# Kernel tuning notes

Hardware: AMD Instinct MI355X
Metric: run time of the kernel (lower is better)

## Reference

```python
import jax, jax.numpy as jnp
import numpy as np

NUM_ENTITIES = 100000
NUM_TIMES = 10000
D = 512
DB = 768
NUM_REL = 200
NUM_BASES = 4
N_NODES = 30000
N_EDGES = 200000
B = 128
P_ENT = 64
P_TIME = 32
T_UNIQ = 2000


def setup_inputs() -> dict:
    key = jax.random.key(0)
    ks = jax.random.split(key, 32)
    n = jax.random.normal
    ri = jax.random.randint
    inp = {}
    # learned params
    inp['emb'] = n(ks[0], (NUM_ENTITIES + NUM_TIMES, D), jnp.float32) * 0.05
    sc = 1.0 / np.sqrt(D)
    inp['basis1'] = n(ks[1], (NUM_BASES, D, D), jnp.float32) * sc
    inp['att1'] = n(ks[2], (NUM_REL, NUM_BASES), jnp.float32) * 0.5
    inp['root1'] = n(ks[3], (D, D), jnp.float32) * sc
    inp['bias1'] = jnp.zeros((D,), jnp.float32)
    inp['basis2'] = n(ks[4], (NUM_BASES, D, D), jnp.float32) * sc
    inp['att2'] = n(ks[5], (NUM_REL, NUM_BASES), jnp.float32) * 0.5
    inp['root2'] = n(ks[6], (D, D), jnp.float32) * sc
    inp['bias2'] = jnp.zeros((D,), jnp.float32)
    sb = 1.0 / np.sqrt(DB)
    inp['W_lin'] = n(ks[7], (DB, D), jnp.float32) * sb
    inp['b_lin'] = jnp.zeros((D,), jnp.float32)
    inp['W_attn'] = n(ks[8], (DB, D), jnp.float32) * sb
    inp['b_attn'] = jnp.zeros((D,), jnp.float32)
    inp['W_prob'] = n(ks[9], (DB, 1), jnp.float32) * sb
    inp['b_prob'] = jnp.zeros((1,), jnp.float32)
    # forward tensor args
    inp['ques_emb_bert'] = n(ks[10], (B, DB), jnp.float32)
    inp['x_idx'] = ri(ks[11], (N_NODES,), 0, NUM_ENTITIES, jnp.int32)
    inp['edge_index'] = ri(ks[12], (2, N_EDGES), 0, N_NODES, jnp.int32)
    inp['edge_type'] = ri(ks[13], (N_EDGES,), 0, NUM_REL, jnp.int32)
    inp['start_time'] = ri(ks[14], (N_EDGES,), 0, NUM_TIMES, jnp.int32)
    inp['end_time'] = ri(ks[15], (N_EDGES,), 0, NUM_TIMES, jnp.int32)
    inp['edge_batch_idx'] = jnp.sort(ri(ks[16], (N_EDGES,), 0, B, jnp.int32))
    inp['edge_norm'] = jax.random.uniform(ks[17], (N_EDGES,), jnp.float32)
    inp['uniq_times'] = ri(ks[18], (T_UNIQ,), 0, NUM_TIMES, jnp.int32)
    # padded index vectors: positions >= count point at the appended zero row
    ent_counts = ri(ks[19], (B,), 1, P_ENT + 1, jnp.int32)
    time_counts = ri(ks[20], (B,), 1, P_TIME + 1, jnp.int32)
    pe = ri(ks[21], (B, P_ENT), 0, N_NODES, jnp.int32)
    pt = ri(ks[22], (B, P_TIME), 0, T_UNIQ, jnp.int32)
    inp['padded_ent'] = jnp.where(jnp.arange(P_ENT)[None, :] < ent_counts[:, None], pe, N_NODES)
    inp['padded_time'] = jnp.where(jnp.arange(P_TIME)[None, :] < time_counts[:, None], pt, T_UNIQ)
    inp['ent_counts'] = ent_counts
    inp['time_counts'] = time_counts
    return inp


def rgcn_layer(x, basis, att, root, bias, src, dst, etype, st_emb, et_emb, q_t, edge_norm):
    # basis decomposition: project all nodes through each basis once. [N, NB, D]
    xb = jnp.einsum('ni,bio->nbo', x, basis)
    coeff = att[etype]                                 # [E, NB]
    msg = jnp.einsum('eb,ebd->ed', coeff, xb[src])     # [E, D]
    # time gate: question-time embedding vs edge interval midpoint embedding
    gate = jax.nn.sigmoid(jnp.sum(q_t * 0.5 * (st_emb + et_emb), axis=-1))  # [E]
    msg = msg * (gate * edge_norm)[:, None]
    agg = jax.ops.segment_sum(msg, dst, num_segments=N_NODES)
    return agg + x @ root + bias


def reference(emb, basis1, att1, root1, bias1, basis2, att2, root2, bias2,
              W_lin, b_lin, W_attn, b_attn, W_prob, b_prob,
              ques_emb_bert, x_idx, edge_index, edge_type, start_time, end_time,
              edge_batch_idx, edge_norm, uniq_times, padded_ent, padded_time,
              ent_counts, time_counts):
    question_embedding = ques_emb_bert @ W_lin + b_lin                  # [B, D]
    time_for_edge_attn = (ques_emb_bert @ W_attn + b_attn)[edge_batch_idx]  # [E, D]
    st_emb = emb[start_time + NUM_ENTITIES]
    et_emb = emb[end_time + NUM_ENTITIES]
    x = emb[x_idx]                                                      # [N, D]
    src, dst = edge_index[0], edge_index[1]
    h = jax.nn.relu(rgcn_layer(x, basis1, att1, root1, bias1, src, dst, edge_type,
                               st_emb, et_emb, time_for_edge_attn, edge_norm))
    # dropout is identity in eval mode
    h = rgcn_layer(h, basis2, att2, root2, bias2, src, dst, edge_type,
                   st_emb, et_emb, time_for_edge_attn, edge_norm)       # [N, D]
    subgraph_time_emb = emb[uniq_times + NUM_ENTITIES]                  # [T_u, D]
    zero = jnp.zeros((1, D), h.dtype)
    ent_w_zeros = jnp.concatenate([h, zero], axis=0)
    time_w_zeros = jnp.concatenate([subgraph_time_emb, zero], axis=0)
    pooled_ent = jnp.sum(ent_w_zeros[padded_ent], axis=1) / ent_counts[:, None].astype(h.dtype)
    pooled_time = jnp.sum(time_w_zeros[padded_time], axis=1) / time_counts[:, None].astype(h.dtype)
    p_ent = jax.nn.sigmoid(ques_emb_bert @ W_prob + b_prob)             # [B, 1]
    pred = (question_embedding + pooled_ent * p_ent + pooled_time * (1.0 - p_ent)) / 3.0
    # batched cosine similarity against full entity+time vocab
    pred_n = pred / jnp.maximum(jnp.linalg.norm(pred, axis=-1, keepdims=True), 1e-8)
    emb_n = emb / jnp.maximum(jnp.linalg.norm(emb, axis=-1, keepdims=True), 1e-8)
    score = pred_n @ emb_n.T                                            # [B, V]
    return score * 30.0
```

## Files before the change

### kernel.cpp

```cpp
#include <hip/hip_runtime.h>

#define NUM_ENT   100000
#define NTIMES    10000
#define DD        512
#define DB        768
#define NREL      200
#define NBAS      4
#define NN        30000
#define NEDGE     200000
#define BATCH     128
#define PENT      64
#define PTIME     32
#define TUNIQ     2000
#define V_TOT     110000
#define V_PAD     110208
#define VT16      6888
#define M_PAD2    30208
#define MT2R      1888
#define KT_L      80
#define KT_E      16
#define PACKB_BLKS 1280
#define GATH_BLKS  7500

typedef __attribute__((ext_vector_type(8))) short s8v;
typedef __attribute__((ext_vector_type(4))) float f4v;

__device__ __forceinline__ unsigned short f2bf(float x){
  unsigned int u = __builtin_bit_cast(unsigned int, x);
  u += 0x7fffu + ((u >> 16) & 1u);
  return (unsigned short)(u >> 16);
}
__device__ __forceinline__ float bf2f(unsigned short h){
  unsigned int u = ((unsigned int)h) << 16;
  return __builtin_bit_cast(float, u);
}

__device__ __forceinline__ void gload16(const void* g, void* l){
  __builtin_amdgcn_global_load_lds(
      (const __attribute__((address_space(1))) void*)g,
      (__attribute__((address_space(3))) void*)l, 16, 0, 0);
}


__global__ __launch_bounds__(256) void k_prep(const float* __restrict__ emb,
    const float* __restrict__ basis1, const float* __restrict__ root1,
    const float* __restrict__ basis2, const float* __restrict__ root2,
    const int* __restrict__ x_idx,
    unsigned short* __restrict__ Bp, float* __restrict__ invn,
    unsigned short* __restrict__ B1p, unsigned short* __restrict__ B2p,
    unsigned short* __restrict__ Ap, unsigned short* __restrict__ x_rm){
  int bid = blockIdx.x;
  if (bid < VT16){
    int vt = bid;
    int wid = threadIdx.x >> 6, lane = threadIdx.x & 63;
    int vrow = vt * 16 + (lane & 15);
    float ss = 0.f;
    __shared__ float ssw[4][16];
    for (int i = 0; i < 4; ++i){
      int kt = wid + i * 4;
      int k0 = kt * 32 + (lane >> 4) * 8;
      s8v o;
      if (vrow < V_TOT){
        const float4* p = reinterpret_cast<const float4*>(emb + (size_t)vrow * DD + k0);
        float4 v0 = p[0], v1 = p[1];
        ss += v0.x*v0.x + v0.y*v0.y + v0.z*v0.z + v0.w*v0.w;
        ss += v1.x*v1.x + v1.y*v1.y + v1.z*v1.z + v1.w*v1.w;
        o[0] = (short)f2bf(v0.x); o[1] = (short)f2bf(v0.y);
        o[2] = (short)f2bf(v0.z); o[3] = (short)f2bf(v0.w);
        o[4] = (short)f2bf(v1.x); o[5] = (short)f2bf(v1.y);
        o[6] = (short)f2bf(v1.z); o[7] = (short)f2bf(v1.w);
      } else {
        #pragma unroll
        for (int j = 0; j < 8; ++j) o[j] = 0;
      }
      *reinterpret_cast<s8v*>(Bp + ((size_t)(kt * VT16 + vt) << 9) + lane * 8) = o;
    }
    ss += __shfl_xor(ss, 16);
    ss += __shfl_xor(ss, 32);
    if ((lane >> 4) == 0) ssw[wid][lane] = ss;
    __syncthreads();
    if (threadIdx.x < 16){
      float s = ssw[0][threadIdx.x] + ssw[1][threadIdx.x] + ssw[2][threadIdx.x] + ssw[3][threadIdx.x];
      int v = vt * 16 + threadIdx.x;
      invn[v] = (v < V_TOT) ? (1.0f / fmaxf(sqrtf(s), 1e-8f)) : 0.0f;
    }
  } else if (bid < VT16 + PACKB_BLKS){
    int idx = (bid - VT16) * 256 + threadIdx.x;
    int set = idx >= KT_L * 32 * 64;
    if (set) idx -= KT_L * 32 * 64;
    const float* basis = set ? basis2 : basis1;
    const float* root  = set ? root2  : root1;
    unsigned short* Bw = set ? B2p : B1p;
    int lane = idx & 63; int kt = idx >> 11;
    int k0 = kt * 32 + (lane >> 4) * 8;
    int col = ((idx >> 6) & 31) * 16 + (lane & 15);
    s8v o;
    #pragma unroll
    for (int j = 0; j < 8; ++j){
      int k = k0 + j;
      float v = (k < 2048) ? basis[(size_t)k * 512 + col] : root[(size_t)(k - 2048) * 512 + col];
      o[j] = (short)f2bf(v);
    }
    *reinterpret_cast<s8v*>(Bw + (size_t)idx * 8) = o;
  } else {
    int gb = bid - (VT16 + PACKB_BLKS);
    int w = (int)((gb * 256 + threadIdx.x) >> 6);
    int lane = threadIdx.x & 63;
    if (w >= NN) return;
    int v = x_idx[w];
    const float4* p = reinterpret_cast<const float4*>(emb + (size_t)v * 512 + lane * 8);
    float4 a = p[0], b = p[1];
    s8v x;
    x[0] = (short)f2bf(a.x); x[1] = (short)f2bf(a.y); x[2] = (short)f2bf(a.z); x[3] = (short)f2bf(a.w);
    x[4] = (short)f2bf(b.x); x[5] = (short)f2bf(b.y); x[6] = (short)f2bf(b.z); x[7] = (short)f2bf(b.w);
    *reinterpret_cast<s8v*>(x_rm + (size_t)w * 512 + lane * 8) = x;
    *reinterpret_cast<s8v*>(Ap + ((size_t)(w >> 4) * KT_L + 64 + (lane >> 2)) * 512
                               + ((w & 15) + (lane & 3) * 16) * 8) = x;
  }
}

__global__ __launch_bounds__(256) void k_small2(const float* __restrict__ ques,
    const float* __restrict__ Wl, const float* __restrict__ bl,
    const float* __restrict__ Wa, const float* __restrict__ ba,
    const float* __restrict__ Wp, const float* __restrict__ bp,
    float* __restrict__ qlin, unsigned short* __restrict__ Apq,
    float* __restrict__ pent){
  if (blockIdx.x == 32){
    int b = threadIdx.x >> 1, half = threadIdx.x & 1;
    float a = 0.f;
    int k0 = half * 384;
    for (int k = k0; k < k0 + 384; ++k)
      a = fmaf(ques[(size_t)b * DB + k], Wp[k], a);
    a += __shfl_xor(a, 1);
    if (half == 0) pent[b] = 1.f / (1.f + expf(-(a + bp[0])));
    return;
  }
  __shared__ float sq[128 * 96];
  int col = threadIdx.x & 31, bg = threadIdx.x >> 5;
  int c0 = blockIdx.x * 32;
  const float* W = (c0 < 512) ? Wl : Wa;
  int wcol = (c0 & 511) + col;
  float acc[16] = {};
  for (int k0 = 0; k0 < DB; k0 += 96){
    __syncthreads();
    for (int i = threadIdx.x; i < 128 * 96; i += 256){
      int b = i / 96, kk = i - b * 96;
      sq[i] = ques[(size_t)b * DB + k0 + kk];
    }
    __syncthreads();
    for (int kk = 0; kk < 96; kk += 4){
      float w0 = W[(size_t)(k0 + kk + 0) * 512 + wcol];
      float w1 = W[(size_t)(k0 + kk + 1) * 512 + wcol];
      float w2 = W[(size_t)(k0 + kk + 2) * 512 + wcol];
      float w3 = W[(size_t)(k0 + kk + 3) * 512 + wcol];
      #pragma unroll
      for (int bb = 0; bb < 16; ++bb){
        float4 qv = *reinterpret_cast<const float4*>(&sq[(bg * 16 + bb) * 96 + kk]);
        acc[bb] = fmaf(qv.x, w0, fmaf(qv.y, w1, fmaf(qv.z, w2, fmaf(qv.w, w3, acc[bb]))));
      }
    }
  }
  if (c0 < 512){
    #pragma unroll
    for (int bb = 0; bb < 16; ++bb)
      qlin[(size_t)(bg * 16 + bb) * 512 + wcol] = acc[bb] + bl[wcol];
  } else {
    float bb_ = ba[wcol];
    size_t base = ((size_t)bg * 16 + (wcol >> 5)) * 512
                + ((wcol >> 3) & 3) * 128 + (wcol & 7);
    #pragma unroll
    for (int bb = 0; bb < 16; ++bb){
      int w = bg * 16 + bb;
      Apq[base + (w & 15) * 8] = f2bf(acc[bb] + bb_);
    }
  }
}

__global__ __launch_bounds__(256) void k_gemm_m2(
    const unsigned short* __restrict__ A, const unsigned short* __restrict__ B,
    float* __restrict__ outf){
  __shared__ __align__(1024) short sAll[3 * 8192];
  const int Kt = KT_E;
  int tid = threadIdx.x;
  int lane = tid & 63, wid = tid >> 6;
  int wr = wid >> 1, wc = wid & 1;
  int rt0 = blockIdx.x * 8;
  int ct0 = blockIdx.y * 8;
  const unsigned short* pA0 = A + ((size_t)(rt0 + 2 * wid) * Kt) * 512 + lane * 8;
  const unsigned short* pA1 = pA0 + (size_t)Kt * 512;
  const unsigned short* pB0 = B + (size_t)(ct0 + 2 * wid) * 512 + lane * 8;
  const unsigned short* pB1 = pB0 + 512;
  size_t gbs = (size_t)VT16 * 512;
  int so = 2 * wid * 512;
  f4v acc[4][4] = {};

  auto STAGE = [&](int buf, int kt){
    short* b = &sAll[buf * 8192];
    gload16(pA0 + (size_t)kt * 512, b + so);
    gload16(pA1 + (size_t)kt * 512, b + so + 512);
    gload16(pB0 + (size_t)kt * gbs, b + 4096 + so);
    gload16(pB1 + (size_t)kt * gbs, b + 4096 + so + 512);
  };
  auto COMPUTE = [&](int buf){
    const short* base = &sAll[buf * 8192];
    s8v af[4], bfr[4];
    #pragma unroll
    for (int m = 0; m < 4; ++m) af[m] = *reinterpret_cast<const s8v*>(base + (wr * 4 + m) * 512 + lane * 8);
    #pragma unroll
    for (int n = 0; n < 4; ++n) bfr[n] = *reinterpret_cast<const s8v*>(base + 4096 + (wc * 4 + n) * 512 + lane * 8);
    #pragma unroll
    for (int m = 0; m < 4; ++m)
      #pragma unroll
      for (int n = 0; n < 4; ++n)
        acc[m][n] = __builtin_amdgcn_mfma_f32_16x16x32_bf16(af[m], bfr[n], acc[m][n], 0, 0, 0);
  };

  STAGE(0, 0);
  STAGE(1, 1);
  int cb = 0, sb = 2;
  for (int kt = 0; kt < Kt - 2; ++kt){
    STAGE(sb, kt + 2);
    asm volatile("s_waitcnt vmcnt(8)" ::: "memory");
    __builtin_amdgcn_s_barrier();
    __builtin_amdgcn_sched_barrier(0);
    COMPUTE(cb);
    __builtin_amdgcn_s_barrier();
    cb = (cb == 2) ? 0 : cb + 1;
    sb = (sb == 2) ? 0 : sb + 1;
  }
  asm volatile("s_waitcnt vmcnt(4)" ::: "memory");
  __builtin_amdgcn_s_barrier();
  __builtin_amdgcn_sched_barrier(0);
  COMPUTE(cb);
  cb = (cb == 2) ? 0 : cb + 1;
  asm volatile("s_waitcnt vmcnt(0)" ::: "memory");
  __builtin_amdgcn_s_barrier();
  __builtin_amdgcn_sched_barrier(0);
  COMPUTE(cb);

  #pragma unroll
  for (int m = 0; m < 4; ++m)
    #pragma unroll
    for (int n = 0; n < 4; ++n){
      int row0 = rt0 * 16 + (wr * 4 + m) * 16 + ((lane >> 4) * 4);
      int col  = (ct0 + wc * 4 + n) * 16 + (lane & 15);
      #pragma unroll
      for (int r = 0; r < 4; ++r){
        int rr = row0 + r;
        if (col < NTIMES) outf[(size_t)rr * NTIMES + col] = acc[m][n][r];
      }
    }
}

__global__ __launch_bounds__(256, 3) void k_score_p(
    const unsigned short* __restrict__ Apred, const unsigned short* __restrict__ Bp,
    const float* __restrict__ invn, float* __restrict__ out){
  __shared__ __align__(1024) short sAll[3 * 8192];
  const int Kt = KT_E;
  int tid = threadIdx.x;
  int lane = tid & 63, wid = tid >> 6;
  int wr = wid >> 1, wc = wid & 1;
  int kq = lane >> 4, r16 = lane & 15;
  int ct0 = blockIdx.x * 8;
  const unsigned short* pA0 = Apred + ((size_t)(2 * wid) * Kt) * 512 + lane * 8;
  const unsigned short* pA1 = pA0 + (size_t)Kt * 512;
  const unsigned short* pB0 = Bp + (size_t)(ct0 + 2 * wid) * 512 + lane * 8;
  const unsigned short* pB1 = pB0 + 512;
  size_t gbs = (size_t)VT16 * 512;
  int so = 2 * wid * 512;
  f4v acc[4][4] = {};

  auto STAGE = [&](int buf, int kt){
    short* b = &sAll[buf * 8192];
    gload16(pA0 + (size_t)kt * 512, b + so);
    gload16(pA1 + (size_t)kt * 512, b + so + 512);
    gload16(pB0 + (size_t)kt * gbs, b + 4096 + so);
    gload16(pB1 + (size_t)kt * gbs, b + 4096 + so + 512);
  };
  auto COMPUTE = [&](int buf){
    const short* base = &sAll[buf * 8192];
    s8v af[4], bfr[4];
    #pragma unroll
    for (int m = 0; m < 4; ++m) af[m] = *reinterpret_cast<const s8v*>(base + (wr * 4 + m) * 512 + lane * 8);
    #pragma unroll
    for (int n = 0; n < 4; ++n) bfr[n] = *reinterpret_cast<const s8v*>(base + 4096 + (wc * 4 + n) * 512 + lane * 8);
    #pragma unroll
    for (int m = 0; m < 4; ++m)
      #pragma unroll
      for (int n = 0; n < 4; ++n)
        acc[m][n] = __builtin_amdgcn_mfma_f32_16x16x32_bf16(af[m], bfr[n], acc[m][n], 0, 0, 0);
  };

  STAGE(0, 0);
  STAGE(1, 1);
  int cb = 0, sb = 2;
  for (int kt = 0; kt < Kt - 2; ++kt){
    STAGE(sb, kt + 2);
    asm volatile("s_waitcnt vmcnt(8)" ::: "memory");
    __builtin_amdgcn_s_barrier();
    __builtin_amdgcn_sched_barrier(0);
    COMPUTE(cb);
    __builtin_amdgcn_s_barrier();
    cb = (cb == 2) ? 0 : cb + 1;
    sb = (sb == 2) ? 0 : sb + 1;
  }
  asm volatile("s_waitcnt vmcnt(4)" ::: "memory");
  __builtin_amdgcn_s_barrier();
  __builtin_amdgcn_sched_barrier(0);
  COMPUTE(cb);
  cb = (cb == 2) ? 0 : cb + 1;
  asm volatile("s_waitcnt vmcnt(0)" ::: "memory");
  __builtin_amdgcn_s_barrier();
  __builtin_amdgcn_sched_barrier(0);
  COMPUTE(cb);

  __syncthreads();
  float* scratch = reinterpret_cast<float*>(sAll) + wid * 2176;
  int colg = ct0 * 16 + wc * 64 + r16 * 4;
  bool c_ok = colg < V_TOT;
  float4 inv4 = float4{0.f, 0.f, 0.f, 0.f};
  if (c_ok){
    inv4 = *reinterpret_cast<const float4*>(invn + colg);
    inv4.x *= 30.f; inv4.y *= 30.f; inv4.z *= 30.f; inv4.w *= 30.f;
  }
  #pragma unroll
  for (int p = 0; p < 2; ++p){
    #pragma unroll
    for (int mm = 0; mm < 2; ++mm){
      int m = p * 2 + mm;
      #pragma unroll
      for (int n = 0; n < 4; ++n)
        #pragma unroll
        for (int r = 0; r < 4; ++r)
          scratch[(mm * 16 + kq * 4 + r) * 68 + n * 16 + r16] = acc[m][n][r];
    }
    #pragma unroll
    for (int i = 0; i < 8; ++i){
      int row_r = i * 4 + kq;
      float4 v = *reinterpret_cast<const float4*>(scratch + row_r * 68 + r16 * 4);
      if (c_ok){
        float4 o;
        o.x = v.x * inv4.x; o.y = v.y * inv4.y; o.z = v.z * inv4.z; o.w = v.w * inv4.w;
        int grr = wr * 64 + p * 32 + row_r;
        *reinterpret_cast<float4*>(out + (size_t)grr * V_TOT + colg) = o;
      }
    }
  }
}

template<int MODE>
__global__ __launch_bounds__(512, 2) void k_gemm512(
    const unsigned short* __restrict__ A, const unsigned short* __restrict__ B,
    const float* __restrict__ bias, unsigned short* __restrict__ outh,
    unsigned short* __restrict__ Ap_tail){
  __shared__ __align__(1024) short sAll[3 * 20480];
  const int Kt = KT_L;
  int tid = threadIdx.x;
  int lane = tid & 63, wid = tid >> 6;
  int wr = wid >> 2, wc = wid & 3;
  int blk = blockIdx.x;
  int rt0 = blk * 8;
  const unsigned short* pA = A + ((size_t)(rt0 + wid) * Kt) * 512 + lane * 8;
  const unsigned short* pB = B + (size_t)(wid * 4) * 512 + lane * 8;
  int soA = wid * 512;
  int soB = 4096 + wid * 4 * 512;
  f4v acc[4][8] = {};

  auto STAGE = [&](int buf, int kt){
    short* b = &sAll[buf * 20480];
    gload16(pA + (size_t)kt * 512, b + soA);
    const unsigned short* pb = pB + (size_t)kt * 32 * 512;
    gload16(pb,        b + soB);
    gload16(pb +  512, b + soB +  512);
    gload16(pb + 1024, b + soB + 1024);
    gload16(pb + 1536, b + soB + 1536);
  };
  auto COMPUTE = [&](int buf){
    const short* base = &sAll[buf * 20480];
    s8v af[4], bfr[8];
    #pragma unroll
    for (int m = 0; m < 4; ++m) af[m] = *reinterpret_cast<const s8v*>(base + (wr * 4 + m) * 512 + lane * 8);
    #pragma unroll
    for (int n = 0; n < 8; ++n) bfr[n] = *reinterpret_cast<const s8v*>(base + 4096 + (wc * 8 + n) * 512 + lane * 8);
    __builtin_amdgcn_s_setprio(1);
    #pragma unroll
    for (int m = 0; m < 4; ++m)
      #pragma unroll
      for (int n = 0; n < 8; ++n)
        acc[m][n] = __builtin_amdgcn_mfma_f32_16x16x32_bf16(af[m], bfr[n], acc[m][n], 0, 0, 0);
    __builtin_amdgcn_s_setprio(0);
  };

  STAGE(0, 0);
  STAGE(1, 1);
  int cb = 0, sb = 2;
  for (int kt = 0; kt < Kt - 2; ++kt){
    STAGE(sb, kt + 2);
    asm volatile("s_waitcnt vmcnt(10)" ::: "memory");
    __builtin_amdgcn_s_barrier();
    __builtin_amdgcn_sched_barrier(0);
    COMPUTE(cb);
    __builtin_amdgcn_s_barrier();
    cb = (cb == 2) ? 0 : cb + 1;
    sb = (sb == 2) ? 0 : sb + 1;
  }
  asm volatile("s_waitcnt vmcnt(5)" ::: "memory");
  __builtin_amdgcn_s_barrier();
  __builtin_amdgcn_sched_barrier(0);
  COMPUTE(cb);
  cb = (cb == 2) ? 0 : cb + 1;
  asm volatile("s_waitcnt vmcnt(0)" ::: "memory");
  __builtin_amdgcn_s_barrier();
  __builtin_amdgcn_sched_barrier(0);
  COMPUTE(cb);

  int R0 = blk * 128 + wr * 64 + ((lane >> 4) * 4);
  int C0 = wc * 128 + (lane & 15);
  #pragma unroll
  for (int m = 0; m < 4; ++m)
    #pragma unroll
    for (int r4 = 0; r4 < 4; ++r4){
      int rr = R0 + m * 16 + r4;
      if (rr < NN){
        #pragma unroll
        for (int n = 0; n < 8; ++n){
          int col = C0 + n * 16;
          float v = acc[m][n][r4] + bias[col];
          if constexpr (MODE == 1){
            v = fmaxf(v, 0.f);
            unsigned short hv = f2bf(v);
            outh[(size_t)rr * 512 + col] = hv;
            Ap_tail[((size_t)(rr >> 4) * KT_L + 64 + (col >> 5)) * 512
                    + ((rr & 15) + ((col >> 3) & 3) * 16) * 8 + (col & 7)] = hv;
          } else {
            outh[(size_t)rr * 512 + col] = f2bf(v);
          }
        }
      }
    }
}

__global__ __launch_bounds__(256) void k_edgeprep(const int* __restrict__ ebatch,
    const int* __restrict__ st, const int* __restrict__ et,
    const float* __restrict__ enorm, const float* __restrict__ M2,
    const int* __restrict__ ei,
    float* __restrict__ we, int* __restrict__ cnt, int* __restrict__ lists){
  int e = blockIdx.x * 256 + threadIdx.x;
  if (e >= NEDGE) return;
  int b = ebatch[e];
  float s = 0.5f * (M2[(size_t)b * NTIMES + st[e]] + M2[(size_t)b * NTIMES + et[e]]);
  we[e] = (1.f / (1.f + expf(-s))) * enorm[e];
  int dst = ei[NEDGE + e];
  int slot = atomicAdd(&cnt[dst], 1);
  if (slot < 64) lists[(size_t)dst * 64 + slot] = e;
}

__global__ __launch_bounds__(256) void k_edge_agg(const unsigned short* __restrict__ xsrc,
    const int* __restrict__ ei, const int* __restrict__ etype,
    const float* __restrict__ we, const float* __restrict__ att,
    const int* __restrict__ cnt, const int* __restrict__ lists,
    unsigned short* __restrict__ Ap){
  __shared__ float satt[NREL * NBAS];
  __shared__ int sed[4][64];
  for (int i = threadIdx.x; i < NREL * NBAS; i += 256) satt[i] = att[i];
  int wid = threadIdx.x >> 6, lane = threadIdx.x & 63;
  int n = blockIdx.x * 4 + wid;
  int deg = min(cnt[n], 64);
  int eid = (lane < deg) ? lists[(size_t)n * 64 + lane] : 0x7fffffff;
  int rank = 0;
  for (int j = 0; j < 64; ++j){
    int v = __shfl(eid, j);
    rank += (v < eid) ? 1 : 0;
  }
  __syncthreads();
  if (lane < deg) sed[wid][rank] = eid;
  __syncthreads();
  float acc[NBAS][8] = {};
  if (deg > 0){
    int my_e = sed[wid][(lane < deg) ? lane : 0];
    int my_s = ei[my_e];
    int my_t = etype[my_e];
    float my_w = we[my_e];
    float c0l = my_w * satt[my_t * 4 + 0];
    float c1l = my_w * satt[my_t * 4 + 1];
    float c2l = my_w * satt[my_t * 4 + 2];
    float c3l = my_w * satt[my_t * 4 + 3];
    int s0 = __shfl(my_s, 0);
    s8v xv = *reinterpret_cast<const s8v*>(xsrc + (size_t)s0 * 512 + lane * 8);
    for (int j = 0; j < deg; ++j){
      s8v xn = xv;
      if (j + 1 < deg){
        int sn = __shfl(my_s, j + 1);
        xn = *reinterpret_cast<const s8v*>(xsrc + (size_t)sn * 512 + lane * 8);
      }
      float c0 = __shfl(c0l, j), c1 = __shfl(c1l, j);
      float c2 = __shfl(c2l, j), c3 = __shfl(c3l, j);
      #pragma unroll
      for (int jj = 0; jj < 8; ++jj){
        float x = bf2f((unsigned short)xv[jj]);
        acc[0][jj] = fmaf(c0, x, acc[0][jj]);
        acc[1][jj] = fmaf(c1, x, acc[1][jj]);
        acc[2][jj] = fmaf(c2, x, acc[2][jj]);
        acc[3][jj] = fmaf(c3, x, acc[3][jj]);
      }
      xv = xn;
    }
  }
  #pragma unroll
  for (int b = 0; b < NBAS; ++b){
    s8v o;
    #pragma unroll
    for (int jj = 0; jj < 8; ++jj) o[jj] = (short)f2bf(acc[b][jj]);
    *reinterpret_cast<s8v*>(Ap + ((size_t)(n >> 4) * KT_L + b * 16 + (lane >> 2)) * 512
                               + ((n & 15) + (lane & 3) * 16) * 8) = o;
  }
}

__global__ __launch_bounds__(256) void k_pred(const unsigned short* __restrict__ h2,
    const float* __restrict__ emb, const int* __restrict__ uniq,
    const int* __restrict__ pent_idx, const int* __restrict__ ptime_idx,
    const int* __restrict__ ent_c, const int* __restrict__ time_c,
    const float* __restrict__ qlin, const float* __restrict__ pent,
    unsigned short* __restrict__ Ap_pred){
  __shared__ float sacc[4][512];
  int b = blockIdx.x;
  int wid = threadIdx.x >> 6, lane = threadIdx.x & 63;
  float a[8] = {};
  if (wid < 2){
    for (int j = wid * 32; j < wid * 32 + 32; ++j){
      int idx = pent_idx[b * PENT + j];
      if (idx < NN){
        s8v hv = *reinterpret_cast<const s8v*>(h2 + (size_t)idx * 512 + lane * 8);
        #pragma unroll
        for (int jj = 0; jj < 8; ++jj) a[jj] += bf2f((unsigned short)hv[jj]);
      }
    }
  } else {
    for (int j = (wid - 2) * 16; j < (wid - 2) * 16 + 16; ++j){
      int ti = ptime_idx[b * PTIME + j];
      if (ti < TUNIQ){
        const float* p = emb + (size_t)(NUM_ENT + uniq[ti]) * 512 + lane * 8;
        #pragma unroll
        for (int jj = 0; jj < 8; ++jj) a[jj] += p[jj];
      }
    }
  }
  #pragma unroll
  for (int jj = 0; jj < 8; ++jj) sacc[wid][lane * 8 + jj] = a[jj];
  __syncthreads();
  if (wid == 0){
    float ce = 1.f / (float)ent_c[b], ct = 1.f / (float)time_c[b];
    float p = pent[b];
    float pr[8]; float ss = 0.f;
    #pragma unroll
    for (int jj = 0; jj < 8; ++jj){
      int i = lane * 8 + jj;
      float ae = sacc[0][i] + sacc[1][i];
      float at = sacc[2][i] + sacc[3][i];
      float v = (qlin[(size_t)b * 512 + i] + ae * ce * p + at * ct * (1.f - p)) * (1.f / 3.f);
      pr[jj] = v; ss += v * v;
    }
    ss += __shfl_xor(ss, 32); ss += __shfl_xor(ss, 16); ss += __shfl_xor(ss, 8);
    ss += __shfl_xor(ss, 4);  ss += __shfl_xor(ss, 2);  ss += __shfl_xor(ss, 1);
    float inv = 1.f / fmaxf(sqrtf(ss), 1e-8f);
    s8v o;
    #pragma unroll
    for (int jj = 0; jj < 8; ++jj) o[jj] = (short)f2bf(pr[jj] * inv);
    *reinterpret_cast<s8v*>(Ap_pred + ((size_t)((b >> 4) * KT_E + (lane >> 2)) << 9)
                                    + ((b & 15) + (lane & 3) * 16) * 8) = o;
  }
}

extern "C" void kernel_launch(void* const* d_in, const int* in_sizes, int n_in,
                              void* d_out, int out_size, void* d_ws, size_t ws_size,
                              hipStream_t stream){
  const float* emb    = (const float*)d_in[0];
  const float* basis1 = (const float*)d_in[1];
  const float* att1   = (const float*)d_in[2];
  const float* root1  = (const float*)d_in[3];
  const float* bias1  = (const float*)d_in[4];
  const float* basis2 = (const float*)d_in[5];
  const float* att2   = (const float*)d_in[6];
  const float* root2  = (const float*)d_in[7];
  const float* bias2  = (const float*)d_in[8];
  const float* W_lin  = (const float*)d_in[9];
  const float* b_lin  = (const float*)d_in[10];
  const float* W_attn = (const float*)d_in[11];
  const float* b_attn = (const float*)d_in[12];
  const float* W_prob = (const float*)d_in[13];
  const float* b_prob = (const float*)d_in[14];
  const float* ques   = (const float*)d_in[15];
  const int* x_idx    = (const int*)d_in[16];
  const int* eidx     = (const int*)d_in[17];
  const int* etype    = (const int*)d_in[18];
  const int* stime    = (const int*)d_in[19];
  const int* etime    = (const int*)d_in[20];
  const int* ebatch   = (const int*)d_in[21];
  const float* enorm  = (const float*)d_in[22];
  const int* uniq     = (const int*)d_in[23];
  const int* pent_i   = (const int*)d_in[24];
  const int* ptime_i  = (const int*)d_in[25];
  const int* ent_c    = (const int*)d_in[26];
  const int* time_c   = (const int*)d_in[27];
  float* out = (float*)d_out;

  char* w = (char*)d_ws;
  size_t off = 0;
  auto alloc = [&](size_t bytes)->char*{ char* p = w + off; off += (bytes + 255) & ~(size_t)255; return p; };
  unsigned short* Bp_emb = (unsigned short*)alloc((size_t)KT_E * VT16 * 1024);
  float*          invn   = (float*)alloc((size_t)V_PAD * 4);
  unsigned short* Ap   = (unsigned short*)alloc((size_t)MT2R * KT_L * 1024);
  unsigned short* B1p  = (unsigned short*)alloc((size_t)KT_L * 32 * 1024);
  unsigned short* B2p  = (unsigned short*)alloc((size_t)KT_L * 32 * 1024);
  char* xh_base = alloc((size_t)NN * 512 * 2 * 2);
  unsigned short* x_rm = (unsigned short*)xh_base;
  unsigned short* h1   = (unsigned short*)(xh_base + (size_t)NN * 512 * 2);
  unsigned short* h2   = (unsigned short*)xh_base;
  float* M2    = (float*)alloc((size_t)BATCH * NTIMES * 4);
  float* we    = (float*)alloc((size_t)NEDGE * 4);
  float* qlin  = (float*)alloc((size_t)BATCH * 512 * 4);
  float* pent  = (float*)alloc(1024);
  unsigned short* Apq    = (unsigned short*)alloc((size_t)8 * KT_E * 1024);
  unsigned short* Appred = (unsigned short*)alloc((size_t)8 * KT_E * 1024);
  int* cnt   = (int*)alloc((size_t)NN * 4);
  int* lists = (int*)alloc((size_t)NN * 64 * 4);
  (void)ws_size; (void)in_sizes; (void)n_in; (void)out_size;

  k_prep<<<VT16 + PACKB_BLKS + GATH_BLKS, 256, 0, stream>>>(
      emb, basis1, root1, basis2, root2, x_idx,
      Bp_emb, invn, B1p, B2p, Ap, x_rm);
  k_small2<<<33, 256, 0, stream>>>(ques, W_lin, b_lin, W_attn, b_attn, W_prob, b_prob,
                                   qlin, Apq, pent);
  k_gemm_m2<<<dim3(1, 79), 256, 0, stream>>>(Apq, Bp_emb + (size_t)6250 * 512, M2);
  hipMemsetAsync(cnt, 0, (size_t)NN * 4, stream);
  k_edgeprep<<<(NEDGE + 255) / 256, 256, 0, stream>>>(ebatch, stime, etime, enorm, M2,
                                                      eidx, we, cnt, lists);
  k_edge_agg<<<NN / 4, 256, 0, stream>>>(x_rm, eidx, etype, we, att1, cnt, lists, Ap);
  k_gemm512<1><<<236, 512, 0, stream>>>(Ap, B1p, bias1, h1, Ap);
  k_edge_agg<<<NN / 4, 256, 0, stream>>>(h1, eidx, etype, we, att2, cnt, lists, Ap);
  k_gemm512<2><<<236, 512, 0, stream>>>(Ap, B2p, bias2, h2, nullptr);
  k_pred<<<BATCH, 256, 0, stream>>>(h2, emb, uniq, pent_i, ptime_i, ent_c, time_c,
                                    qlin, pent, Appred);
  k_score_p<<<861, 256, 0, stream>>>(Appred, Bp_emb, invn, out);
}
```

Baseline: 676.9 us.

## Drop row-major activation copies and gather edge sources from tiled GEMM buffer

The gather and layer-1 GEMM no longer write separate row-major bf16 copies of the node features (x_rm and h1). Edge aggregation instead reads source rows straight from the tiled tail of the GEMM A buffer. This removes two full N×D bf16 write streams and a workspace buffer. In exchange, each edge now gathers its row as 16-byte pieces spread across 16 tiles rather than one contiguous 1 KB row, which may coalesce worse. Separately, the vocab packing step now reads embedding rows contiguously, transposes them through shared memory, and computes norms from the bf16-rounded values.

```diff
diff --git a/kernel.cpp b/kernel.cpp
--- a/kernel.cpp
+++ b/kernel.cpp
@@ -48,23 +48,21 @@
     const int* __restrict__ x_idx,
     unsigned short* __restrict__ Bp, float* __restrict__ invn,
     unsigned short* __restrict__ B1p, unsigned short* __restrict__ B2p,
-    unsigned short* __restrict__ Ap, unsigned short* __restrict__ x_rm){
+    unsigned short* __restrict__ Ap){
+  __shared__ unsigned short srow[16][520];
+  __shared__ float ssw[4][16];
   int bid = blockIdx.x;
   if (bid < VT16){
     int vt = bid;
     int wid = threadIdx.x >> 6, lane = threadIdx.x & 63;
-    int vrow = vt * 16 + (lane & 15);
-    float ss = 0.f;
-    __shared__ float ssw[4][16];
+    #pragma unroll
     for (int i = 0; i < 4; ++i){
-      int kt = wid + i * 4;
-      int k0 = kt * 32 + (lane >> 4) * 8;
+      int r = wid * 4 + i;
+      int vrow = vt * 16 + r;
       s8v o;
       if (vrow < V_TOT){
-        const float4* p = reinterpret_cast<const float4*>(emb + (size_t)vrow * DD + k0);
+        const float4* p = reinterpret_cast<const float4*>(emb + (size_t)vrow * DD + lane * 8);
         float4 v0 = p[0], v1 = p[1];
-        ss += v0.x*v0.x + v0.y*v0.y + v0.z*v0.z + v0.w*v0.w;
-        ss += v1.x*v1.x + v1.y*v1.y + v1.z*v1.z + v1.w*v1.w;
         o[0] = (short)f2bf(v0.x); o[1] = (short)f2bf(v0.y);
         o[2] = (short)f2bf(v0.z); o[3] = (short)f2bf(v0.w);
         o[4] = (short)f2bf(v1.x); o[5] = (short)f2bf(v1.y);
@@ -73,11 +71,22 @@
         #pragma unroll
         for (int j = 0; j < 8; ++j) o[j] = 0;
       }
+      *reinterpret_cast<s8v*>(&srow[r][lane * 8]) = o;
+    }
+    __syncthreads();
+    float ss = 0.f;
+    int r16 = lane & 15, kq = lane >> 4;
+    #pragma unroll
+    for (int i = 0; i < 4; ++i){
+      int kt = wid + i * 4;
+      s8v o = *reinterpret_cast<const s8v*>(&srow[r16][kt * 32 + kq * 8]);
+      #pragma unroll
+      for (int j = 0; j < 8; ++j){ float x = bf2f((unsigned short)o[j]); ss = fmaf(x, x, ss); }
       *reinterpret_cast<s8v*>(Bp + ((size_t)(kt * VT16 + vt) << 9) + lane * 8) = o;
     }
     ss += __shfl_xor(ss, 16);
     ss += __shfl_xor(ss, 32);
-    if ((lane >> 4) == 0) ssw[wid][lane] = ss;
+    if (kq == 0) ssw[wid][r16] = ss;
     __syncthreads();
     if (threadIdx.x < 16){
       float s = ssw[0][threadIdx.x] + ssw[1][threadIdx.x] + ssw[2][threadIdx.x] + ssw[3][threadIdx.x];
@@ -113,7 +122,6 @@
     s8v x;
     x[0] = (short)f2bf(a.x); x[1] = (short)f2bf(a.y); x[2] = (short)f2bf(a.z); x[3] = (short)f2bf(a.w);
     x[4] = (short)f2bf(b.x); x[5] = (short)f2bf(b.y); x[6] = (short)f2bf(b.z); x[7] = (short)f2bf(b.w);
-    *reinterpret_cast<s8v*>(x_rm + (size_t)w * 512 + lane * 8) = x;
     *reinterpret_cast<s8v*>(Ap + ((size_t)(w >> 4) * KT_L + 64 + (lane >> 2)) * 512
                                + ((w & 15) + (lane & 3) * 16) * 8) = x;
   }
@@ -428,10 +436,8 @@
           float v = acc[m][n][r4] + bias[col];
           if constexpr (MODE == 1){
             v = fmaxf(v, 0.f);
-            unsigned short hv = f2bf(v);
-            outh[(size_t)rr * 512 + col] = hv;
             Ap_tail[((size_t)(rr >> 4) * KT_L + 64 + (col >> 5)) * 512
-                    + ((rr & 15) + ((col >> 3) & 3) * 16) * 8 + (col & 7)] = hv;
+                    + ((rr & 15) + ((col >> 3) & 3) * 16) * 8 + (col & 7)] = f2bf(v);
           } else {
             outh[(size_t)rr * 512 + col] = f2bf(v);
           }
@@ -455,7 +461,7 @@
   if (slot < 64) lists[(size_t)dst * 64 + slot] = e;
 }
 
-__global__ __launch_bounds__(256) void k_edge_agg(const unsigned short* __restrict__ xsrc,
+__global__ __launch_bounds__(256) void k_edge_agg(
     const int* __restrict__ ei, const int* __restrict__ etype,
     const float* __restrict__ we, const float* __restrict__ att,
     const int* __restrict__ cnt, const int* __restrict__ lists,
@@ -475,6 +481,8 @@
   __syncthreads();
   if (lane < deg) sed[wid][rank] = eid;
   __syncthreads();
+  int tl_kt = 64 + (lane >> 2);
+  int tl_sub = (lane & 3) * 16;
   float acc[NBAS][8] = {};
   if (deg > 0){
     int my_e = sed[wid][(lane < deg) ? lane : 0];
@@ -485,13 +493,17 @@
     float c1l = my_w * satt[my_t * 4 + 1];
     float c2l = my_w * satt[my_t * 4 + 2];
     float c3l = my_w * satt[my_t * 4 + 3];
+    auto tailld = [&](int s)->s8v{
+      return *reinterpret_cast<const s8v*>(
+          Ap + ((size_t)(s >> 4) * KT_L + tl_kt) * 512 + ((s & 15) + tl_sub) * 8);
+    };
     int s0 = __shfl(my_s, 0);
-    s8v xv = *reinterpret_cast<const s8v*>(xsrc + (size_t)s0 * 512 + lane * 8);
+    s8v xv = tailld(s0);
     for (int j = 0; j < deg; ++j){
       s8v xn = xv;
       if (j + 1 < deg){
         int sn = __shfl(my_s, j + 1);
-        xn = *reinterpret_cast<const s8v*>(xsrc + (size_t)sn * 512 + lane * 8);
+        xn = tailld(sn);
       }
       float c0 = __shfl(c0l, j), c1 = __shfl(c1l, j);
       float c2 = __shfl(c2l, j), c3 = __shfl(c3l, j);
@@ -612,10 +624,7 @@
   unsigned short* Ap   = (unsigned short*)alloc((size_t)MT2R * KT_L * 1024);
   unsigned short* B1p  = (unsigned short*)alloc((size_t)KT_L * 32 * 1024);
   unsigned short* B2p  = (unsigned short*)alloc((size_t)KT_L * 32 * 1024);
-  char* xh_base = alloc((size_t)NN * 512 * 2 * 2);
-  unsigned short* x_rm = (unsigned short*)xh_base;
-  unsigned short* h1   = (unsigned short*)(xh_base + (size_t)NN * 512 * 2);
-  unsigned short* h2   = (unsigned short*)xh_base;
+  unsigned short* h2   = (unsigned short*)alloc((size_t)NN * 512 * 2);
   float* M2    = (float*)alloc((size_t)BATCH * NTIMES * 4);
   float* we    = (float*)alloc((size_t)NEDGE * 4);
   float* qlin  = (float*)alloc((size_t)BATCH * 512 * 4);
@@ -628,16 +637,16 @@
 
   k_prep<<<VT16 + PACKB_BLKS + GATH_BLKS, 256, 0, stream>>>(
       emb, basis1, root1, basis2, root2, x_idx,
-      Bp_emb, invn, B1p, B2p, Ap, x_rm);
+      Bp_emb, invn, B1p, B2p, Ap);
   k_small2<<<33, 256, 0, stream>>>(ques, W_lin, b_lin, W_attn, b_attn, W_prob, b_prob,
                                    qlin, Apq, pent);
   k_gemm_m2<<<dim3(1, 79), 256, 0, stream>>>(Apq, Bp_emb + (size_t)6250 * 512, M2);
   hipMemsetAsync(cnt, 0, (size_t)NN * 4, stream);
   k_edgeprep<<<(NEDGE + 255) / 256, 256, 0, stream>>>(ebatch, stime, etime, enorm, M2,
                                                       eidx, we, cnt, lists);
-  k_edge_agg<<<NN / 4, 256, 0, stream>>>(x_rm, eidx, etype, we, att1, cnt, lists, Ap);
-  k_gemm512<1><<<236, 512, 0, stream>>>(Ap, B1p, bias1, h1, Ap);
-  k_edge_agg<<<NN / 4, 256, 0, stream>>>(h1, eidx, etype, we, att2, cnt, lists, Ap);
+  k_edge_agg<<<NN / 4, 256, 0, stream>>>(eidx, etype, we, att1, cnt, lists, Ap);
+  k_gemm512<1><<<236, 512, 0, stream>>>(Ap, B1p, bias1, nullptr, Ap);
+  k_edge_agg<<<NN / 4, 256, 0, stream>>>(eidx, etype, we, att2, cnt, lists, Ap);
   k_gemm512<2><<<236, 512, 0, stream>>>(Ap, B2p, bias2, h2, nullptr);
   k_pred<<<BATCH, 256, 0, stream>>>(h2, emb, uniq, pent_i, ptime_i, ent_c, time_c,
                                     qlin, pent, Appred);
```

New measurement: 1.040 ms. 53.7% more time.

## Switch GEMM operands from pre-tiled fragment layout to row-major buffers

Applied to the files above, without the earlier changes.

The pre-packed MFMA-tile layouts for the embedding table, the RGCN weight and activation matrices, and the query/pred vectors are replaced with plain row-major (or column-transposed) buffers. The GEMM kernels now stage tiles by gathering 16 rows with strided 16-byte loads. This also drops duplicate stores: x_rm and h1 are no longer written separately from the packed A matrix, and the norm reduction becomes per-row wave shuffles. The tradeoff is that the tile loads are less contiguous than the previous fully packed 1KB chunks, which may cost memory efficiency in the score and layer GEMMs.

```diff
diff --git a/kernel.cpp b/kernel.cpp
--- a/kernel.cpp
+++ b/kernel.cpp
@@ -14,9 +14,9 @@
 #define TUNIQ     2000
 #define V_TOT     110000
 #define V_PAD     110208
-#define VT16      6888
+#define VCONV     6888
 #define M_PAD2    30208
-#define MT2R      1888
+#define KL        2560
 #define KT_L      80
 #define KT_E      16
 #define PACKB_BLKS 1280
@@ -46,25 +46,22 @@
     const float* __restrict__ basis1, const float* __restrict__ root1,
     const float* __restrict__ basis2, const float* __restrict__ root2,
     const int* __restrict__ x_idx,
-    unsigned short* __restrict__ Bp, float* __restrict__ invn,
-    unsigned short* __restrict__ B1p, unsigned short* __restrict__ B2p,
-    unsigned short* __restrict__ Ap, unsigned short* __restrict__ x_rm){
+    unsigned short* __restrict__ Eb, float* __restrict__ invn,
+    unsigned short* __restrict__ Bt1, unsigned short* __restrict__ Bt2,
+    unsigned short* __restrict__ Az){
   int bid = blockIdx.x;
-  if (bid < VT16){
-    int vt = bid;
-    int wid = threadIdx.x >> 6, lane = threadIdx.x & 63;
-    int vrow = vt * 16 + (lane & 15);
-    float ss = 0.f;
-    __shared__ float ssw[4][16];
+  int wid = threadIdx.x >> 6, lane = threadIdx.x & 63;
+  if (bid < VCONV){
+    #pragma unroll
     for (int i = 0; i < 4; ++i){
-      int kt = wid + i * 4;
-      int k0 = kt * 32 + (lane >> 4) * 8;
+      int row = bid * 16 + wid * 4 + i;
       s8v o;
-      if (vrow < V_TOT){
-        const float4* p = reinterpret_cast<const float4*>(emb + (size_t)vrow * DD + k0);
+      float ss = 0.f;
+      if (row < V_TOT){
+        const float4* p = reinterpret_cast<const float4*>(emb + (size_t)row * DD + lane * 8);
         float4 v0 = p[0], v1 = p[1];
-        ss += v0.x*v0.x + v0.y*v0.y + v0.z*v0.z + v0.w*v0.w;
-        ss += v1.x*v1.x + v1.y*v1.y + v1.z*v1.z + v1.w*v1.w;
+        ss = v0.x*v0.x + v0.y*v0.y + v0.z*v0.z + v0.w*v0.w
+           + v1.x*v1.x + v1.y*v1.y + v1.z*v1.z + v1.w*v1.w;
         o[0] = (short)f2bf(v0.x); o[1] = (short)f2bf(v0.y);
         o[2] = (short)f2bf(v0.z); o[3] = (short)f2bf(v0.w);
         o[4] = (short)f2bf(v1.x); o[5] = (short)f2bf(v1.y);
@@ -73,27 +70,22 @@
         #pragma unroll
         for (int j = 0; j < 8; ++j) o[j] = 0;
       }
-      *reinterpret_cast<s8v*>(Bp + ((size_t)(kt * VT16 + vt) << 9) + lane * 8) = o;
-    }
-    ss += __shfl_xor(ss, 16);
-    ss += __shfl_xor(ss, 32);
-    if ((lane >> 4) == 0) ssw[wid][lane] = ss;
-    __syncthreads();
-    if (threadIdx.x < 16){
-      float s = ssw[0][threadIdx.x] + ssw[1][threadIdx.x] + ssw[2][threadIdx.x] + ssw[3][threadIdx.x];
-      int v = vt * 16 + threadIdx.x;
-      invn[v] = (v < V_TOT) ? (1.0f / fmaxf(sqrtf(s), 1e-8f)) : 0.0f;
-    }
-  } else if (bid < VT16 + PACKB_BLKS){
-    int idx = (bid - VT16) * 256 + threadIdx.x;
-    int set = idx >= KT_L * 32 * 64;
-    if (set) idx -= KT_L * 32 * 64;
+      *reinterpret_cast<s8v*>(Eb + (size_t)row * 512 + lane * 8) = o;
+      ss += __shfl_xor(ss, 1);  ss += __shfl_xor(ss, 2);  ss += __shfl_xor(ss, 4);
+      ss += __shfl_xor(ss, 8);  ss += __shfl_xor(ss, 16); ss += __shfl_xor(ss, 32);
+      if (lane == 0)
+        invn[row] = (row < V_TOT) ? (1.0f / fmaxf(sqrtf(ss), 1e-8f)) : 0.0f;
+    }
+  } else if (bid < VCONV + PACKB_BLKS){
+    int wt = (bid - VCONV) * 4 + wid;
+    int set = wt >= 2560;
+    int wt2 = wt - set * 2560;
+    int colg = wt2 / 320, kc = wt2 - colg * 320;
     const float* basis = set ? basis2 : basis1;
     const float* root  = set ? root2  : root1;
-    unsigned short* Bw = set ? B2p : B1p;
-    int lane = idx & 63; int kt = idx >> 11;
-    int k0 = kt * 32 + (lane >> 4) * 8;
-    int col = ((idx >> 6) & 31) * 16 + (lane & 15);
+    unsigned short* Bt = set ? Bt2 : Bt1;
+    int col = colg * 64 + lane;
+    int k0 = kc * 8;
     s8v o;
     #pragma unroll
     for (int j = 0; j < 8; ++j){
@@ -101,11 +93,10 @@
       float v = (k < 2048) ? basis[(size_t)k * 512 + col] : root[(size_t)(k - 2048) * 512 + col];
       o[j] = (short)f2bf(v);
     }
-    *reinterpret_cast<s8v*>(Bw + (size_t)idx * 8) = o;
+    *reinterpret_cast<s8v*>(Bt + (size_t)col * KL + k0) = o;
   } else {
-    int gb = bid - (VT16 + PACKB_BLKS);
+    int gb = bid - (VCONV + PACKB_BLKS);
     int w = (int)((gb * 256 + threadIdx.x) >> 6);
-    int lane = threadIdx.x & 63;
     if (w >= NN) return;
     int v = x_idx[w];
     const float4* p = reinterpret_cast<const float4*>(emb + (size_t)v * 512 + lane * 8);
@@ -113,9 +104,7 @@
     s8v x;
     x[0] = (short)f2bf(a.x); x[1] = (short)f2bf(a.y); x[2] = (short)f2bf(a.z); x[3] = (short)f2bf(a.w);
     x[4] = (short)f2bf(b.x); x[5] = (short)f2bf(b.y); x[6] = (short)f2bf(b.z); x[7] = (short)f2bf(b.w);
-    *reinterpret_cast<s8v*>(x_rm + (size_t)w * 512 + lane * 8) = x;
-    *reinterpret_cast<s8v*>(Ap + ((size_t)(w >> 4) * KT_L + 64 + (lane >> 2)) * 512
-                               + ((w & 15) + (lane & 3) * 16) * 8) = x;
+    *reinterpret_cast<s8v*>(Az + (size_t)w * KL + 2048 + lane * 8) = x;
   }
 }
 
@@ -123,7 +112,7 @@
     const float* __restrict__ Wl, const float* __restrict__ bl,
     const float* __restrict__ Wa, const float* __restrict__ ba,
     const float* __restrict__ Wp, const float* __restrict__ bp,
-    float* __restrict__ qlin, unsigned short* __restrict__ Apq,
+    float* __restrict__ qlin, unsigned short* __restrict__ qat,
     float* __restrict__ pent){
   if (blockIdx.x == 32){
     int b = threadIdx.x >> 1, half = threadIdx.x & 1;
@@ -166,40 +155,36 @@
       qlin[(size_t)(bg * 16 + bb) * 512 + wcol] = acc[bb] + bl[wcol];
   } else {
     float bb_ = ba[wcol];
-    size_t base = ((size_t)bg * 16 + (wcol >> 5)) * 512
-                + ((wcol >> 3) & 3) * 128 + (wcol & 7);
-    #pragma unroll
-    for (int bb = 0; bb < 16; ++bb){
-      int w = bg * 16 + bb;
-      Apq[base + (w & 15) * 8] = f2bf(acc[bb] + bb_);
-    }
+    #pragma unroll
+    for (int bb = 0; bb < 16; ++bb)
+      qat[(size_t)(bg * 16 + bb) * 512 + wcol] = f2bf(acc[bb] + bb_);
   }
 }
 
 __global__ __launch_bounds__(256) void k_gemm_m2(
-    const unsigned short* __restrict__ A, const unsigned short* __restrict__ B,
+    const unsigned short* __restrict__ qat, const unsigned short* __restrict__ Eb,
     float* __restrict__ outf){
   __shared__ __align__(1024) short sAll[3 * 8192];
   const int Kt = KT_E;
   int tid = threadIdx.x;
   int lane = tid & 63, wid = tid >> 6;
   int wr = wid >> 1, wc = wid & 1;
+  int r16 = lane & 15, kq = lane >> 4;
   int rt0 = blockIdx.x * 8;
   int ct0 = blockIdx.y * 8;
-  const unsigned short* pA0 = A + ((size_t)(rt0 + 2 * wid) * Kt) * 512 + lane * 8;
-  const unsigned short* pA1 = pA0 + (size_t)Kt * 512;
-  const unsigned short* pB0 = B + (size_t)(ct0 + 2 * wid) * 512 + lane * 8;
-  const unsigned short* pB1 = pB0 + 512;
-  size_t gbs = (size_t)VT16 * 512;
+  const unsigned short* pA0 = qat + (size_t)((rt0 + 2 * wid) * 16 + r16) * 512 + kq * 8;
+  const unsigned short* pA1 = qat + (size_t)((rt0 + 2 * wid + 1) * 16 + r16) * 512 + kq * 8;
+  const unsigned short* pB0 = Eb + (size_t)(NUM_ENT + (ct0 + 2 * wid) * 16 + r16) * 512 + kq * 8;
+  const unsigned short* pB1 = Eb + (size_t)(NUM_ENT + (ct0 + 2 * wid + 1) * 16 + r16) * 512 + kq * 8;
   int so = 2 * wid * 512;
   f4v acc[4][4] = {};
 
   auto STAGE = [&](int buf, int kt){
     short* b = &sAll[buf * 8192];
-    gload16(pA0 + (size_t)kt * 512, b + so);
-    gload16(pA1 + (size_t)kt * 512, b + so + 512);
-    gload16(pB0 + (size_t)kt * gbs, b + 4096 + so);
-    gload16(pB1 + (size_t)kt * gbs, b + 4096 + so + 512);
+    gload16(pA0 + kt * 32, b + so);
+    gload16(pA1 + kt * 32, b + so + 512);
+    gload16(pB0 + kt * 32, b + 4096 + so);
+    gload16(pB1 + kt * 32, b + 4096 + so + 512);
   };
   auto COMPUTE = [&](int buf){
     const short* base = &sAll[buf * 8192];
@@ -253,7 +238,7 @@
 }
 
 __global__ __launch_bounds__(256, 3) void k_score_p(
-    const unsigned short* __restrict__ Apred, const unsigned short* __restrict__ Bp,
+    const unsigned short* __restrict__ predb, const unsigned short* __restrict__ Eb,
     const float* __restrict__ invn, float* __restrict__ out){
   __shared__ __align__(1024) short sAll[3 * 8192];
   const int Kt = KT_E;
@@ -262,20 +247,19 @@
   int wr = wid >> 1, wc = wid & 1;
   int kq = lane >> 4, r16 = lane & 15;
   int ct0 = blockIdx.x * 8;
-  const unsigned short* pA0 = Apred + ((size_t)(2 * wid) * Kt) * 512 + lane * 8;
-  const unsigned short* pA1 = pA0 + (size_t)Kt * 512;
-  const unsigned short* pB0 = Bp + (size_t)(ct0 + 2 * wid) * 512 + lane * 8;
-  const unsigned short* pB1 = pB0 + 512;
-  size_t gbs = (size_t)VT16 * 512;
+  const unsigned short* pA0 = predb + (size_t)(2 * wid * 16 + r16) * 512 + kq * 8;
+  const unsigned short* pA1 = predb + (size_t)((2 * wid + 1) * 16 + r16) * 512 + kq * 8;
+  const unsigned short* pB0 = Eb + (size_t)((ct0 + 2 * wid) * 16 + r16) * 512 + kq * 8;
+  const unsigned short* pB1 = Eb + (size_t)((ct0 + 2 * wid + 1) * 16 + r16) * 512 + kq * 8;
   int so = 2 * wid * 512;
   f4v acc[4][4] = {};
 
   auto STAGE = [&](int buf, int kt){
     short* b = &sAll[buf * 8192];
-    gload16(pA0 + (size_t)kt * 512, b + so);
-    gload16(pA1 + (size_t)kt * 512, b + so + 512);
-    gload16(pB0 + (size_t)kt * gbs, b + 4096 + so);
-    gload16(pB1 + (size_t)kt * gbs, b + 4096 + so + 512);
+    gload16(pA0 + kt * 32, b + so);
+    gload16(pA1 + kt * 32, b + so + 512);
+    gload16(pB0 + kt * 32, b + 4096 + so);
+    gload16(pB1 + kt * 32, b + 4096 + so + 512);
   };
   auto COMPUTE = [&](int buf){
     const short* base = &sAll[buf * 8192];
@@ -350,30 +334,32 @@
 
 template<int MODE>
 __global__ __launch_bounds__(512, 2) void k_gemm512(
-    const unsigned short* __restrict__ A, const unsigned short* __restrict__ B,
+    const unsigned short* __restrict__ A, const unsigned short* __restrict__ Bt,
     const float* __restrict__ bias, unsigned short* __restrict__ outh,
-    unsigned short* __restrict__ Ap_tail){
+    unsigned short* __restrict__ Az_h){
   __shared__ __align__(1024) short sAll[3 * 20480];
   const int Kt = KT_L;
   int tid = threadIdx.x;
   int lane = tid & 63, wid = tid >> 6;
   int wr = wid >> 2, wc = wid & 3;
+  int r16 = lane & 15, kq = lane >> 4;
   int blk = blockIdx.x;
-  int rt0 = blk * 8;
-  const unsigned short* pA = A + ((size_t)(rt0 + wid) * Kt) * 512 + lane * 8;
-  const unsigned short* pB = B + (size_t)(wid * 4) * 512 + lane * 8;
+  const unsigned short* pA = A + (size_t)(blk * 128 + wid * 16 + r16) * KL + kq * 8;
+  const unsigned short* pB0 = Bt + (size_t)((wid * 4 + 0) * 16 + r16) * KL + kq * 8;
+  const unsigned short* pB1 = Bt + (size_t)((wid * 4 + 1) * 16 + r16) * KL + kq * 8;
+  const unsigned short* pB2 = Bt + (size_t)((wid * 4 + 2) * 16 + r16) * KL + kq * 8;
+  const unsigned short* pB3 = Bt + (size_t)((wid * 4 + 3) * 16 + r16) * KL + kq * 8;
   int soA = wid * 512;
   int soB = 4096 + wid * 4 * 512;
   f4v acc[4][8] = {};
 
   auto STAGE = [&](int buf, int kt){
     short* b = &sAll[buf * 20480];
-    gload16(pA + (size_t)kt * 512, b + soA);
-    const unsigned short* pb = pB + (size_t)kt * 32 * 512;
-    gload16(pb,        b + soB);
-    gload16(pb +  512, b + soB +  512);
-    gload16(pb + 1024, b + soB + 1024);
-    gload16(pb + 1536, b + soB + 1536);
+    gload16(pA  + kt * 32, b + soA);
+    gload16(pB0 + kt * 32, b + soB);
+    gload16(pB1 + kt * 32, b + soB +  512);
+    gload16(pB2 + kt * 32, b + soB + 1024);
+    gload16(pB3 + kt * 32, b + soB + 1536);
   };
   auto COMPUTE = [&](int buf){
     const short* base = &sAll[buf * 20480];
@@ -428,10 +414,7 @@
           float v = acc[m][n][r4] + bias[col];
           if constexpr (MODE == 1){
             v = fmaxf(v, 0.f);
-            unsigned short hv = f2bf(v);
-            outh[(size_t)rr * 512 + col] = hv;
-            Ap_tail[((size_t)(rr >> 4) * KT_L + 64 + (col >> 5)) * 512
-                    + ((rr & 15) + ((col >> 3) & 3) * 16) * 8 + (col & 7)] = hv;
+            Az_h[(size_t)rr * KL + 2048 + col] = f2bf(v);
           } else {
             outh[(size_t)rr * 512 + col] = f2bf(v);
           }
@@ -459,7 +442,7 @@
     const int* __restrict__ ei, const int* __restrict__ etype,
     const float* __restrict__ we, const float* __restrict__ att,
     const int* __restrict__ cnt, const int* __restrict__ lists,
-    unsigned short* __restrict__ Ap){
+    unsigned short* __restrict__ Az){
   __shared__ float satt[NREL * NBAS];
   __shared__ int sed[4][64];
   for (int i = threadIdx.x; i < NREL * NBAS; i += 256) satt[i] = att[i];
@@ -486,12 +469,12 @@
     float c2l = my_w * satt[my_t * 4 + 2];
     float c3l = my_w * satt[my_t * 4 + 3];
     int s0 = __shfl(my_s, 0);
-    s8v xv = *reinterpret_cast<const s8v*>(xsrc + (size_t)s0 * 512 + lane * 8);
+    s8v xv = *reinterpret_cast<const s8v*>(xsrc + (size_t)s0 * KL + lane * 8);
     for (int j = 0; j < deg; ++j){
       s8v xn = xv;
       if (j + 1 < deg){
         int sn = __shfl(my_s, j + 1);
-        xn = *reinterpret_cast<const s8v*>(xsrc + (size_t)sn * 512 + lane * 8);
+        xn = *reinterpret_cast<const s8v*>(xsrc + (size_t)sn * KL + lane * 8);
       }
       float c0 = __shfl(c0l, j), c1 = __shfl(c1l, j);
       float c2 = __shfl(c2l, j), c3 = __shfl(c3l, j);
@@ -511,8 +494,7 @@
     s8v o;
     #pragma unroll
     for (int jj = 0; jj < 8; ++jj) o[jj] = (short)f2bf(acc[b][jj]);
-    *reinterpret_cast<s8v*>(Ap + ((size_t)(n >> 4) * KT_L + b * 16 + (lane >> 2)) * 512
-                               + ((n & 15) + (lane & 3) * 16) * 8) = o;
+    *reinterpret_cast<s8v*>(Az + (size_t)n * KL + b * 512 + lane * 8) = o;
   }
 }
 
@@ -521,7 +503,7 @@
     const int* __restrict__ pent_idx, const int* __restrict__ ptime_idx,
     const int* __restrict__ ent_c, const int* __restrict__ time_c,
     const float* __restrict__ qlin, const float* __restrict__ pent,
-    unsigned short* __restrict__ Ap_pred){
+    unsigned short* __restrict__ predb){
   __shared__ float sacc[4][512];
   int b = blockIdx.x;
   int wid = threadIdx.x >> 6, lane = threadIdx.x & 63;
@@ -566,8 +548,7 @@
     s8v o;
     #pragma unroll
     for (int jj = 0; jj < 8; ++jj) o[jj] = (short)f2bf(pr[jj] * inv);
-    *reinterpret_cast<s8v*>(Ap_pred + ((size_t)((b >> 4) * KT_E + (lane >> 2)) << 9)
-                                    + ((b & 15) + (lane & 3) * 16) * 8) = o;
+    *reinterpret_cast<s8v*>(predb + (size_t)b * 512 + lane * 8) = o;
   }
 }
 
@@ -607,39 +588,36 @@
   char* w = (char*)d_ws;
   size_t off = 0;
   auto alloc = [&](size_t bytes)->char*{ char* p = w + off; off += (bytes + 255) & ~(size_t)255; return p; };
-  unsigned short* Bp_emb = (unsigned short*)alloc((size_t)KT_E * VT16 * 1024);
-  float*          invn   = (float*)alloc((size_t)V_PAD * 4);
-  unsigned short* Ap   = (unsigned short*)alloc((size_t)MT2R * KT_L * 1024);
-  unsigned short* B1p  = (unsigned short*)alloc((size_t)KT_L * 32 * 1024);
-  unsigned short* B2p  = (unsigned short*)alloc((size_t)KT_L * 32 * 1024);
-  char* xh_base = alloc((size_t)NN * 512 * 2 * 2);
-  unsigned short* x_rm = (unsigned short*)xh_base;
-  unsigned short* h1   = (unsigned short*)(xh_base + (size_t)NN * 512 * 2);
-  unsigned short* h2   = (unsigned short*)xh_base;
+  unsigned short* Eb   = (unsigned short*)alloc((size_t)V_PAD * 512 * 2);
+  float*          invn = (float*)alloc((size_t)V_PAD * 4);
+  unsigned short* Az   = (unsigned short*)alloc((size_t)M_PAD2 * KL * 2);
+  unsigned short* Bt1  = (unsigned short*)alloc((size_t)512 * KL * 2);
+  unsigned short* Bt2  = (unsigned short*)alloc((size_t)512 * KL * 2);
+  unsigned short* h2   = (unsigned short*)alloc((size_t)NN * 512 * 2);
   float* M2    = (float*)alloc((size_t)BATCH * NTIMES * 4);
   float* we    = (float*)alloc((size_t)NEDGE * 4);
   float* qlin  = (float*)alloc((size_t)BATCH * 512 * 4);
   float* pent  = (float*)alloc(1024);
-  unsigned short* Apq    = (unsigned short*)alloc((size_t)8 * KT_E * 1024);
-  unsigned short* Appred = (unsigned short*)alloc((size_t)8 * KT_E * 1024);
+  unsigned short* qat   = (unsigned short*)alloc((size_t)BATCH * 512 * 2);
+  unsigned short* predb = (unsigned short*)alloc((size_t)BATCH * 512 * 2);
   int* cnt   = (int*)alloc((size_t)NN * 4);
   int* lists = (int*)alloc((size_t)NN * 64 * 4);
   (void)ws_size; (void)in_sizes; (void)n_in; (void)out_size;
 
-  k_prep<<<VT16 + PACKB_BLKS + GATH_BLKS, 256, 0, stream>>>(
+  k_prep<<<VCONV + PACKB_BLKS + GATH_BLKS, 256, 0, stream>>>(
       emb, basis1, root1, basis2, root2, x_idx,
-      Bp_emb, invn, B1p, B2p, Ap, x_rm);
+      Eb, invn, Bt1, Bt2, Az);
   k_small2<<<33, 256, 0, stream>>>(ques, W_lin, b_lin, W_attn, b_attn, W_prob, b_prob,
-                                   qlin, Apq, pent);
-  k_gemm_m2<<<dim3(1, 79), 256, 0, stream>>>(Apq, Bp_emb + (size_t)6250 * 512, M2);
+                                   qlin, qat, pent);
+  k_gemm_m2<<<dim3(1, 79), 256, 0, stream>>>(qat, Eb, M2);
   hipMemsetAsync(cnt, 0, (size_t)NN * 4, stream);
   k_edgeprep<<<(NEDGE + 255) / 256, 256, 0, stream>>>(ebatch, stime, etime, enorm, M2,
                                                       eidx, we, cnt, lists);
-  k_edge_agg<<<NN / 4, 256, 0, stream>>>(x_rm, eidx, etype, we, att1, cnt, lists, Ap);
-  k_gemm512<1><<<236, 512, 0, stream>>>(Ap, B1p, bias1, h1, Ap);
-  k_edge_agg<<<NN / 4, 256, 0, stream>>>(h1, eidx, etype, we, att2, cnt, lists, Ap);
-  k_gemm512<2><<<236, 512, 0, stream>>>(Ap, B2p, bias2, h2, nullptr);
+  k_edge_agg<<<NN / 4, 256, 0, stream>>>(Az + 2048, eidx, etype, we, att1, cnt, lists, Az);
+  k_gemm512<1><<<236, 512, 0, stream>>>(Az, Bt1, bias1, nullptr, Az);
+  k_edge_agg<<<NN / 4, 256, 0, stream>>>(Az + 2048, eidx, etype, we, att2, cnt, lists, Az);
+  k_gemm512<2><<<236, 512, 0, stream>>>(Az, Bt2, bias2, h2, nullptr);
   k_pred<<<BATCH, 256, 0, stream>>>(h2, emb, uniq, pent_i, ptime_i, ent_c, time_c,
-                                    qlin, pent, Appred);
-  k_score_p<<<861, 256, 0, stream>>>(Appred, Bp_emb, invn, out);
-}
+                                    qlin, pent, predb);
+  k_score_p<<<861, 256, 0, stream>>>(predb, Eb, invn, out);
+}
```

Measured after the change: 669.7 us. Within noise of the previous version (-1.1%).
